# Optimization experiments

Measured on AMD Instinct MI355X. Metric: run time of the kernel, lower is better.

The kernel has to match this reference:

```python
import jax, jax.numpy as jnp
from jax import lax
import numpy as np

EPS = 1e-5
K = 12
S = 32  # sample_point


def sq_dist(q, p):
    # q: [b,m,3], p: [b,n,3] -> [b,m,n]
    return (jnp.sum(q * q, -1)[..., None]
            - 2.0 * jnp.einsum('bmc,bnc->bmn', q, p)
            + jnp.sum(p * p, -1)[:, None, :])


def fps(xyz, m):
    # furthest point sampling, starts at index 0 (matches pointnet2_utils)
    b, n, _ = xyz.shape
    init_idx = jnp.zeros((b,), jnp.int32)

    def step(carry, _):
        dist, last = carry  # dist [b,n], last [b]
        last_xyz = jnp.take_along_axis(xyz, last[:, None, None], axis=1)  # [b,1,3]
        d = jnp.sum((xyz - last_xyz) ** 2, -1)  # [b,n]
        dist = jnp.minimum(dist, d)
        nxt = jnp.argmax(dist, -1).astype(jnp.int32)
        return (dist, nxt), nxt

    (_, _), idxs = lax.scan(step, (jnp.full((b, n), 1e10, xyz.dtype), init_idx), None, length=m - 1)
    return jnp.concatenate([init_idx[None, :], idxs], 0).T  # [b,m]


def index_points(points, idx):
    # points [b,n,c], idx [b,...] -> [b,...,c]
    b = points.shape[0]
    flat = idx.reshape(b, -1)
    g = jnp.take_along_axis(points, flat[..., None], axis=1)
    return g.reshape(idx.shape + (points.shape[-1],))


def knn(k, xyz, new_xyz):
    d = sq_dist(new_xyz, xyz)  # [b,m,n]
    return lax.top_k(-d, k)[1]  # k smallest distances


def graph_op(grouped, W, bias, gamma, beta, mean, var):
    # grouped [b,m,k,d]; pointwise conv (kernel_size=1) + BN(eval) + ReLU + max over k
    y = jnp.einsum('bmkd,od->bmko', grouped, W) + bias
    y = (y - mean) * (gamma * lax.rsqrt(var + EPS)) + beta
    y = jnp.maximum(y, 0.0)
    return jnp.max(y, axis=2)  # [b,m,out]


def setup_inputs() -> dict:
    key = jax.random.key(0)
    ks = jax.random.split(key, 16)
    b, n = 16, 8192
    d_s, d_t, d_out = 256, 1024, 1024
    inp = {
        'feature_s': jax.random.normal(ks[0], (b, n, d_s), jnp.float32),
        'xyz_s': jax.random.uniform(ks[1], (b, n, 3), jnp.float32),
        'feature_t': jax.random.normal(ks[2], (b, n, d_t), jnp.float32),
        'xyz_t': jax.random.uniform(ks[3], (b, n, 3), jnp.float32),
        'Ws': jax.random.normal(ks[4], (d_out, d_s), jnp.float32) * 0.05,
        'bias_s': jax.random.normal(ks[5], (d_out,), jnp.float32) * 0.05,
        'gamma_s': jnp.ones((d_out,), jnp.float32),
        'beta_s': jnp.zeros((d_out,), jnp.float32),
        'mean_s': jax.random.normal(ks[6], (d_out,), jnp.float32) * 0.05,
        'var_s': jax.random.uniform(ks[7], (d_out,), jnp.float32, 0.5, 1.5),
        'Wt': jax.random.normal(ks[8], (d_out, d_t), jnp.float32) * 0.03,
        'bias_t': jax.random.normal(ks[9], (d_out,), jnp.float32) * 0.05,
        'gamma_t': jnp.ones((d_out,), jnp.float32),
        'beta_t': jnp.zeros((d_out,), jnp.float32),
        'mean_t': jax.random.normal(ks[10], (d_out,), jnp.float32) * 0.05,
        'var_t': jax.random.uniform(ks[11], (d_out,), jnp.float32, 0.5, 1.5),
    }
    return inp


def reference(feature_s, xyz_s, feature_t, xyz_t,
              Ws, bias_s, gamma_s, beta_s, mean_s, var_s,
              Wt, bias_t, gamma_t, beta_t, mean_t, var_t):
    # total_xyz defaults to xyz_t
    fps_idx = fps(xyz_t, S)                    # [b,S]
    new_xyz = index_points(xyz_t, fps_idx)     # [b,S,3]
    idx_t = knn(K, xyz_t, new_xyz)             # [b,S,K]
    grouped_t = index_points(feature_t, idx_t) # [b,S,K,1024]
    idx_s = knn(K, xyz_s, new_xyz)             # [b,S,K]
    grouped_s = index_points(feature_s, idx_s) # [b,S,K,256]
    out_s = graph_op(grouped_s, Ws, bias_s, gamma_s, beta_s, mean_s, var_s)
    out_t = graph_op(grouped_t, Wt, bias_t, gamma_t, beta_t, mean_t, var_t)
    return (out_s, out_t)
```

## Files before the change

### kernel.cpp

```cpp
#include <hip/hip_runtime.h>
#include <hip/hip_bf16.h>


#define NPTS 8192
#define SPTS 32
#define KNN_K 12
#define DS 256
#define DT 1024
#define DOUT 1024

typedef float f32x4 __attribute__((ext_vector_type(4)));
typedef __bf16 bf16x8 __attribute__((ext_vector_type(8)));
typedef unsigned short ushort_t;
typedef unsigned long long u64;

__device__ __forceinline__ ushort_t f2bf(float f) {
    unsigned int u = __float_as_uint(f);
    u += 0x7fffu + ((u >> 16) & 1u);
    return (ushort_t)(u >> 16);
}

__global__ __launch_bounds__(512) void fps_convw_kernel(const float* __restrict__ xyz,
                                                        float* __restrict__ new_xyz,
                                                        const float* __restrict__ Wt,
                                                        ushort_t* __restrict__ Wb_t,
                                                        const float* __restrict__ Ws,
                                                        ushort_t* __restrict__ Wb_s) {
    int bid = blockIdx.x;
    int tid = threadIdx.x;

    if (bid >= 16) {
        int lin = (bid - 16) * 512 + tid;
        const int stride = 240 * 512;
        for (int i = lin; i < (DT * DOUT) / 4; i += stride) {
            int col = i >> 8, k4 = i & 255;
            float4 v = reinterpret_cast<const float4*>(Wt)[i];
            ushort4 u;
            u.x = f2bf(v.x); u.y = f2bf(v.y); u.z = f2bf(v.z); u.w = f2bf(v.w);
            size_t off = (size_t)(k4 >> 3) * (DOUT * 32) + col * 32 + (k4 & 7) * 4;
            *reinterpret_cast<ushort4*>(Wb_t + off) = u;
        }
        for (int i = lin; i < (DS * DOUT) / 4; i += stride) {
            int col = i >> 6, k4 = i & 63;
            float4 v = reinterpret_cast<const float4*>(Ws)[i];
            ushort4 u;
            u.x = f2bf(v.x); u.y = f2bf(v.y); u.z = f2bf(v.z); u.w = f2bf(v.w);
            size_t off = (size_t)(k4 >> 3) * (DOUT * 32) + col * 32 + (k4 & 7) * 4;
            *reinterpret_cast<ushort4*>(Wb_s + off) = u;
        }
        return;
    }

    {
#pragma clang fp contract(off)
        int b = bid;
        const float* base = xyz + (size_t)b * NPTS * 3;

        __shared__ float cx[NPTS], cy[NPTS], cz[NPTS];
        __shared__ u64 rkey[2][8];

        float px[16], py[16], pz[16], dd[16];
#pragma unroll
        for (int i = 0; i < 16; ++i) {
            int p = tid + i * 512;
            px[i] = base[p * 3 + 0];
            py[i] = base[p * 3 + 1];
            pz[i] = base[p * 3 + 2];
            dd[i] = 1e10f;
            cx[p] = px[i]; cy[p] = py[i]; cz[p] = pz[i];
        }

        float lx = base[0], ly = base[1], lz = base[2];
        if (tid == 0) {
            new_xyz[((size_t)b * SPTS + 0) * 3 + 0] = lx;
            new_xyz[((size_t)b * SPTS + 0) * 3 + 1] = ly;
            new_xyz[((size_t)b * SPTS + 0) * 3 + 2] = lz;
        }

        int w = tid >> 6;
        for (int it = 1; it < SPTS; ++it) {
            int par = it & 1;
            u64 bk = 0;
#pragma unroll
            for (int i = 0; i < 16; ++i) {
                float dx = px[i] - lx, dy = py[i] - ly, dz = pz[i] - lz;
                float d = dx * dx + dy * dy;
                d = d + dz * dz;
                float nd = fminf(dd[i], d);
                dd[i] = nd;
                u64 kd = ((u64)__float_as_uint(nd) << 32) | (unsigned)(8191 - (tid + i * 512));
                bk = (kd > bk) ? kd : bk;
            }
#pragma unroll
            for (int off = 1; off < 64; off <<= 1) {
                u64 ok = __shfl_xor(bk, off);
                bk = (ok > bk) ? ok : bk;
            }
            if ((tid & 63) == 0) rkey[par][w] = bk;
            __syncthreads();
            u64 nk = rkey[par][0];
#pragma unroll
            for (int w2 = 1; w2 < 8; ++w2) {
                u64 v2 = rkey[par][w2];
                nk = (v2 > nk) ? v2 : nk;
            }
            int idx = 8191 - (int)(unsigned)(nk & 0xFFFFFFFFull);
            lx = cx[idx]; ly = cy[idx]; lz = cz[idx];
            if (tid == 0) {
                new_xyz[((size_t)b * SPTS + it) * 3 + 0] = lx;
                new_xyz[((size_t)b * SPTS + it) * 3 + 1] = ly;
                new_xyz[((size_t)b * SPTS + it) * 3 + 2] = lz;
            }
        }
    }
}

__global__ __launch_bounds__(512) void knn_kernel(const float* __restrict__ xyz_s,
                                                  const float* __restrict__ xyz_t,
                                                  const float* __restrict__ new_xyz,
                                                  int* __restrict__ idx_s,
                                                  int* __restrict__ idx_t) {
#pragma clang fp contract(off)
    int q = blockIdx.x;
    int tid = threadIdx.x;
    int w = tid >> 6, lane = tid & 63;
    int set = w >> 2;
    int sw = w & 3;
    int b = q >> 5;

    const float* pts = (set ? xyz_t : xyz_s) + (size_t)b * NPTS * 3;

    float qx = new_xyz[q * 3 + 0];
    float qy = new_xyz[q * 3 + 1];
    float qz = new_xyz[q * 3 + 2];
    float qq = qx * qx + qy * qy;
    qq = qq + qz * qz;

    u64 bd[12];
#pragma unroll
    for (int j = 0; j < 12; ++j) bd[j] = ~0ULL;

    for (int i = 0; i < 2048 / 64; ++i) {
        int p = sw * 2048 + i * 64 + lane;
        float p0 = pts[p * 3 + 0], p1 = pts[p * 3 + 1], p2 = pts[p * 3 + 2];
        float pp = p0 * p0 + p1 * p1; pp = pp + p2 * p2;
        float dot = qx * p0 + qy * p1; dot = dot + qz * p2;
        float d = (qq - 2.0f * dot) + pp;
        unsigned u = __float_as_uint(d);
        u = (u & 0x80000000u) ? ~u : (u | 0x80000000u);
        u64 key = ((u64)u << 32) | (unsigned)p;
        if (key < bd[11]) {
#pragma unroll
            for (int j = 11; j > 0; --j) {
                bool keep = (key >= bd[j]);
                u64 sh = (key >= bd[j - 1]) ? key : bd[j - 1];
                bd[j] = keep ? bd[j] : sh;
            }
            if (key < bd[0]) bd[0] = key;
        }
    }

    __shared__ u64 sd[2][48];

#pragma unroll
    for (int r = 0; r < KNN_K; ++r) {
        u64 cv = bd[0];
#pragma unroll
        for (int off = 1; off < 64; off <<= 1) {
            u64 ov = __shfl_xor(cv, off);
            cv = (ov < cv) ? ov : cv;
        }
        if (lane == 0) sd[set][sw * KNN_K + r] = cv;
        if (cv == bd[0]) {
#pragma unroll
            for (int j = 0; j < 11; ++j) bd[j] = bd[j + 1];
            bd[11] = ~0ULL;
        }
    }
    __syncthreads();

    if (sw == 0) {
        int* outp = (set ? idx_t : idx_s) + q * KNN_K;
        u64 cd = (lane < 48) ? sd[set][lane] : ~0ULL;
#pragma unroll
        for (int r = 0; r < KNN_K; ++r) {
            u64 mv = cd;
#pragma unroll
            for (int off = 1; off < 64; off <<= 1) {
                u64 ov = __shfl_xor(mv, off);
                mv = (ov < mv) ? ov : mv;
            }
            if (lane == 0) outp[r] = (int)(unsigned)(mv & 0xFFFFFFFFull);
            if (cd == mv) cd = ~0ULL;
        }
    }
}

template <int KD>
__device__ __forceinline__ void gemm_body(int mblk, int ch, const float* __restrict__ feat,
                                          const int* __restrict__ idx,
                                          const ushort_t* __restrict__ Wb,
                                          const float* __restrict__ bias,
                                          const float* __restrict__ gamma,
                                          const float* __restrict__ beta,
                                          const float* __restrict__ mean,
                                          const float* __restrict__ var,
                                          float* __restrict__ out,
                                          ushort_t (*abuf)[64][40]) {
    const int NK = KD / 32;
    int tid = threadIdx.x;
    int w = tid >> 6, lane = tid & 63;
    int lrow = lane & 15, kgrp = lane >> 4;

    int r = tid >> 3, seg = tid & 7;
    int q = mblk * 4 + (r >> 4);
    int k = r & 15;
    bool valid = (k < KNN_K);
    int b = q >> 5;
    int src = valid ? idx[q * KNN_K + k] : 0;
    const float* srcp = feat + ((size_t)b * NPTS + src) * KD + seg * 4;

    f32x4 acc[4][4];
#pragma unroll
    for (int mi = 0; mi < 4; ++mi)
#pragma unroll
        for (int ni = 0; ni < 4; ++ni) {
            f32x4 z = {0.f, 0.f, 0.f, 0.f};
            acc[mi][ni] = z;
        }

    {
        float4 v = {0.f, 0.f, 0.f, 0.f};
        if (valid) v = *reinterpret_cast<const float4*>(srcp);
        ushort4 u;
        u.x = f2bf(v.x); u.y = f2bf(v.y); u.z = f2bf(v.z); u.w = f2bf(v.w);
        *reinterpret_cast<ushort4*>(&abuf[0][r][seg * 4]) = u;
    }
    __syncthreads();

    for (int kk = 0; kk < NK; ++kk) {
        int cur = kk & 1;
        float4 nv = {0.f, 0.f, 0.f, 0.f};
        if (kk + 1 < NK && valid)
            nv = *reinterpret_cast<const float4*>(srcp + (kk + 1) * 32);

        bf16x8 a[4];
#pragma unroll
        for (int mf = 0; mf < 4; ++mf)
            a[mf] = *reinterpret_cast<const bf16x8*>(&abuf[cur][mf * 16 + lrow][kgrp * 8]);

#pragma unroll
        for (int nf = 0; nf < 4; ++nf) {
            int col = ch * 512 + w * 64 + nf * 16 + lrow;
            const ushort_t* bp = Wb + (size_t)kk * (DOUT * 32) + (size_t)col * 32 + kgrp * 8;
            bf16x8 bfr = *reinterpret_cast<const bf16x8*>(bp);
#pragma unroll
            for (int mf = 0; mf < 4; ++mf)
                acc[mf][nf] = __builtin_amdgcn_mfma_f32_16x16x32_bf16(a[mf], bfr, acc[mf][nf], 0, 0, 0);
        }

        if (kk + 1 < NK) {
            ushort4 u;
            u.x = f2bf(nv.x); u.y = f2bf(nv.y); u.z = f2bf(nv.z); u.w = f2bf(nv.w);
            *reinterpret_cast<ushort4*>(&abuf[cur ^ 1][r][seg * 4]) = u;
        }
        __syncthreads();
    }

#pragma unroll
    for (int nf = 0; nf < 4; ++nf) {
        int col = ch * 512 + w * 64 + nf * 16 + lrow;
        float sc = gamma[col] / sqrtf(var[col] + 1e-5f);
        float sh = (bias[col] - mean[col]) * sc + beta[col];
#pragma unroll
        for (int mf = 0; mf < 4; ++mf) {
            float m;
            if (kgrp < 3) {
                float y0 = fmaxf(acc[mf][nf][0] * sc + sh, 0.0f);
                float y1 = fmaxf(acc[mf][nf][1] * sc + sh, 0.0f);
                float y2 = fmaxf(acc[mf][nf][2] * sc + sh, 0.0f);
                float y3 = fmaxf(acc[mf][nf][3] * sc + sh, 0.0f);
                m = fmaxf(fmaxf(y0, y1), fmaxf(y2, y3));
            } else {
                m = -1e30f;
            }
            m = fmaxf(m, __shfl_xor(m, 16));
            m = fmaxf(m, __shfl_xor(m, 32));
            if (kgrp == 0) out[(size_t)(mblk * 4 + mf) * DOUT + col] = m;
        }
    }
}

struct GP {
    const float* feature_s; const float* feature_t;
    const int* idx_s; const int* idx_t;
    const ushort_t* Wb_s; const ushort_t* Wb_t;
    const float* bias_s; const float* gamma_s; const float* beta_s;
    const float* mean_s; const float* var_s;
    const float* bias_t; const float* gamma_t; const float* beta_t;
    const float* mean_t; const float* var_t;
    float* out;
};

__global__ __launch_bounds__(512, 4) void gemm_kernel(GP P) {
    __shared__ ushort_t abuf[2][64][40];
    int bid = blockIdx.x;
    bool is_t = (bid < 256);
    int r2 = bid & 255;
    int mblk = r2 >> 1, ch = r2 & 1;
    if (is_t) {
        gemm_body<DT>(mblk, ch, P.feature_t, P.idx_t, P.Wb_t, P.bias_t, P.gamma_t,
                      P.beta_t, P.mean_t, P.var_t, P.out + (size_t)512 * 1024, abuf);
    } else {
        gemm_body<DS>(mblk, ch, P.feature_s, P.idx_s, P.Wb_s, P.bias_s, P.gamma_s,
                      P.beta_s, P.mean_s, P.var_s, P.out, abuf);
    }
}

extern "C" void kernel_launch(void* const* d_in, const int* in_sizes, int n_in,
                              void* d_out, int out_size, void* d_ws, size_t ws_size,
                              hipStream_t stream) {
    const float* feature_s = (const float*)d_in[0];
    const float* xyz_s     = (const float*)d_in[1];
    const float* feature_t = (const float*)d_in[2];
    const float* xyz_t     = (const float*)d_in[3];
    const float* Ws        = (const float*)d_in[4];
    const float* Wt        = (const float*)d_in[10];
    float* out = (float*)d_out;

    char* ws = (char*)d_ws;
    float* new_xyz  = (float*)(ws + 0);
    int* idx_s      = (int*)(ws + 8192);
    int* idx_t      = (int*)(ws + 32768);
    ushort_t* Wb_s  = (ushort_t*)(ws + 57344);
    ushort_t* Wb_t  = (ushort_t*)(ws + 581632);

    fps_convw_kernel<<<256, 512, 0, stream>>>(xyz_t, new_xyz, Wt, Wb_t, Ws, Wb_s);
    knn_kernel<<<512, 512, 0, stream>>>(xyz_s, xyz_t, new_xyz, idx_s, idx_t);

    GP P;
    P.feature_s = feature_s; P.feature_t = feature_t;
    P.idx_s = idx_s; P.idx_t = idx_t;
    P.Wb_s = Wb_s; P.Wb_t = Wb_t;
    P.bias_s = (const float*)d_in[5];  P.gamma_s = (const float*)d_in[6];
    P.beta_s = (const float*)d_in[7];  P.mean_s  = (const float*)d_in[8];
    P.var_s  = (const float*)d_in[9];
    P.bias_t = (const float*)d_in[11]; P.gamma_t = (const float*)d_in[12];
    P.beta_t = (const float*)d_in[13]; P.mean_t  = (const float*)d_in[14];
    P.var_t  = (const float*)d_in[15];
    P.out = out;

    gemm_kernel<<<512, 512, 0, stream>>>(P);
}
```

Baseline: 108.6 us.

## Restructure grouped GEMM to one query per block without shared memory staging

The GEMM kernel now gives each block one query and a 256-column slice, and each wave loads its 12 gathered feature rows straight from global memory into MFMA A fragments. This removes the LDS double buffer and the block-wide syncs. Conversion to bf16 now uses the packed v_cvt_pk_bf16_f32 instruction, and the grid grows to 4096 blocks of 256 threads. In exchange, weight fragments are no longer reused across four queries, so weight traffic rises about fourfold and A rows are reloaded by every wave and column tile.

```diff
diff --git a/kernel.cpp b/kernel.cpp
--- a/kernel.cpp
+++ b/kernel.cpp
@@ -197,7 +197,7 @@
 }
 
 template <int KD>
-__device__ __forceinline__ void gemm_body(int mblk, int ch, const float* __restrict__ feat,
+__device__ __forceinline__ void gemm_wave(int q, int ct, const float* __restrict__ feat,
                                           const int* __restrict__ idx,
                                           const ushort_t* __restrict__ Wb,
                                           const float* __restrict__ bias,
@@ -205,89 +205,64 @@
                                           const float* __restrict__ beta,
                                           const float* __restrict__ mean,
                                           const float* __restrict__ var,
-                                          float* __restrict__ out,
-                                          ushort_t (*abuf)[64][40]) {
+                                          float* __restrict__ out) {
     const int NK = KD / 32;
     int tid = threadIdx.x;
     int w = tid >> 6, lane = tid & 63;
     int lrow = lane & 15, kgrp = lane >> 4;
-
-    int r = tid >> 3, seg = tid & 7;
-    int q = mblk * 4 + (r >> 4);
-    int k = r & 15;
-    bool valid = (k < KNN_K);
     int b = q >> 5;
-    int src = valid ? idx[q * KNN_K + k] : 0;
-    const float* srcp = feat + ((size_t)b * NPTS + src) * KD + seg * 4;
-
-    f32x4 acc[4][4];
-#pragma unroll
-    for (int mi = 0; mi < 4; ++mi)
-#pragma unroll
-        for (int ni = 0; ni < 4; ++ni) {
-            f32x4 z = {0.f, 0.f, 0.f, 0.f};
-            acc[mi][ni] = z;
-        }
-
-    {
-        float4 v = {0.f, 0.f, 0.f, 0.f};
-        if (valid) v = *reinterpret_cast<const float4*>(srcp);
-        ushort4 u;
-        u.x = f2bf(v.x); u.y = f2bf(v.y); u.z = f2bf(v.z); u.w = f2bf(v.w);
-        *reinterpret_cast<ushort4*>(&abuf[0][r][seg * 4]) = u;
-    }
-    __syncthreads();
-
+
+    int rl = (lrow < KNN_K) ? lrow : 0;
+    int src = idx[q * KNN_K + rl];
+    const float* ap = feat + ((size_t)b * NPTS + src) * KD + kgrp * 8;
+    int colbase = ct * 256 + w * 64;
+
+    f32x4 acc[4];
+#pragma unroll
+    for (int nf = 0; nf < 4; ++nf) {
+        f32x4 z = {0.f, 0.f, 0.f, 0.f};
+        acc[nf] = z;
+    }
+
+#pragma unroll 4
     for (int kk = 0; kk < NK; ++kk) {
-        int cur = kk & 1;
-        float4 nv = {0.f, 0.f, 0.f, 0.f};
-        if (kk + 1 < NK && valid)
-            nv = *reinterpret_cast<const float4*>(srcp + (kk + 1) * 32);
-
-        bf16x8 a[4];
-#pragma unroll
-        for (int mf = 0; mf < 4; ++mf)
-            a[mf] = *reinterpret_cast<const bf16x8*>(&abuf[cur][mf * 16 + lrow][kgrp * 8]);
-
+        float4 alo = *reinterpret_cast<const float4*>(ap + kk * 32);
+        float4 ahi = *reinterpret_cast<const float4*>(ap + kk * 32 + 4);
+        unsigned w0, w1, w2, w3;
+        asm("v_cvt_pk_bf16_f32 %0, %1, %2" : "=v"(w0) : "v"(alo.x), "v"(alo.y));
+        asm("v_cvt_pk_bf16_f32 %0, %1, %2" : "=v"(w1) : "v"(alo.z), "v"(alo.w));
+        asm("v_cvt_pk_bf16_f32 %0, %1, %2" : "=v"(w2) : "v"(ahi.x), "v"(ahi.y));
+        asm("v_cvt_pk_bf16_f32 %0, %1, %2" : "=v"(w3) : "v"(ahi.z), "v"(ahi.w));
+        union { unsigned u[4]; bf16x8 v; } au;
+        au.u[0] = w0; au.u[1] = w1; au.u[2] = w2; au.u[3] = w3;
+        bf16x8 af = au.v;
+
+        const ushort_t* bp = Wb + (size_t)kk * (DOUT * 32) + (size_t)(colbase + lrow) * 32 + kgrp * 8;
 #pragma unroll
         for (int nf = 0; nf < 4; ++nf) {
-            int col = ch * 512 + w * 64 + nf * 16 + lrow;
-            const ushort_t* bp = Wb + (size_t)kk * (DOUT * 32) + (size_t)col * 32 + kgrp * 8;
-            bf16x8 bfr = *reinterpret_cast<const bf16x8*>(bp);
-#pragma unroll
-            for (int mf = 0; mf < 4; ++mf)
-                acc[mf][nf] = __builtin_amdgcn_mfma_f32_16x16x32_bf16(a[mf], bfr, acc[mf][nf], 0, 0, 0);
-        }
-
-        if (kk + 1 < NK) {
-            ushort4 u;
-            u.x = f2bf(nv.x); u.y = f2bf(nv.y); u.z = f2bf(nv.z); u.w = f2bf(nv.w);
-            *reinterpret_cast<ushort4*>(&abuf[cur ^ 1][r][seg * 4]) = u;
-        }
-        __syncthreads();
+            bf16x8 bfr = *reinterpret_cast<const bf16x8*>(bp + nf * 512);
+            acc[nf] = __builtin_amdgcn_mfma_f32_16x16x32_bf16(af, bfr, acc[nf], 0, 0, 0);
+        }
     }
 
 #pragma unroll
     for (int nf = 0; nf < 4; ++nf) {
-        int col = ch * 512 + w * 64 + nf * 16 + lrow;
+        int col = colbase + nf * 16 + lrow;
         float sc = gamma[col] / sqrtf(var[col] + 1e-5f);
         float sh = (bias[col] - mean[col]) * sc + beta[col];
-#pragma unroll
-        for (int mf = 0; mf < 4; ++mf) {
-            float m;
-            if (kgrp < 3) {
-                float y0 = fmaxf(acc[mf][nf][0] * sc + sh, 0.0f);
-                float y1 = fmaxf(acc[mf][nf][1] * sc + sh, 0.0f);
-                float y2 = fmaxf(acc[mf][nf][2] * sc + sh, 0.0f);
-                float y3 = fmaxf(acc[mf][nf][3] * sc + sh, 0.0f);
-                m = fmaxf(fmaxf(y0, y1), fmaxf(y2, y3));
-            } else {
-                m = -1e30f;
-            }
-            m = fmaxf(m, __shfl_xor(m, 16));
-            m = fmaxf(m, __shfl_xor(m, 32));
-            if (kgrp == 0) out[(size_t)(mblk * 4 + mf) * DOUT + col] = m;
-        }
+        float m;
+        if (kgrp < 3) {
+            float y0 = fmaxf(acc[nf][0] * sc + sh, 0.0f);
+            float y1 = fmaxf(acc[nf][1] * sc + sh, 0.0f);
+            float y2 = fmaxf(acc[nf][2] * sc + sh, 0.0f);
+            float y3 = fmaxf(acc[nf][3] * sc + sh, 0.0f);
+            m = fmaxf(fmaxf(y0, y1), fmaxf(y2, y3));
+        } else {
+            m = -1e30f;
+        }
+        m = fmaxf(m, __shfl_xor(m, 16));
+        m = fmaxf(m, __shfl_xor(m, 32));
+        if (kgrp == 0) out[(size_t)q * DOUT + col] = m;
     }
 }
 
@@ -302,18 +277,17 @@
     float* out;
 };
 
-__global__ __launch_bounds__(512, 4) void gemm_kernel(GP P) {
-    __shared__ ushort_t abuf[2][64][40];
+__global__ __launch_bounds__(256, 6) void gemm_kernel(GP P) {
     int bid = blockIdx.x;
-    bool is_t = (bid < 256);
-    int r2 = bid & 255;
-    int mblk = r2 >> 1, ch = r2 & 1;
+    bool is_t = (bid < 2048);
+    int r2 = bid & 2047;
+    int q = r2 >> 2, ct = r2 & 3;
     if (is_t) {
-        gemm_body<DT>(mblk, ch, P.feature_t, P.idx_t, P.Wb_t, P.bias_t, P.gamma_t,
-                      P.beta_t, P.mean_t, P.var_t, P.out + (size_t)512 * 1024, abuf);
+        gemm_wave<DT>(q, ct, P.feature_t, P.idx_t, P.Wb_t, P.bias_t, P.gamma_t,
+                      P.beta_t, P.mean_t, P.var_t, P.out + (size_t)512 * 1024);
     } else {
-        gemm_body<DS>(mblk, ch, P.feature_s, P.idx_s, P.Wb_s, P.bias_s, P.gamma_s,
-                      P.beta_s, P.mean_s, P.var_s, P.out, abuf);
+        gemm_wave<DS>(q, ct, P.feature_s, P.idx_s, P.Wb_s, P.bias_s, P.gamma_s,
+                      P.beta_s, P.mean_s, P.var_s, P.out);
     }
 }
 
@@ -350,5 +324,5 @@
     P.var_t  = (const float*)d_in[15];
     P.out = out;
 
-    gemm_kernel<<<512, 512, 0, stream>>>(P);
-}
+    gemm_kernel<<<4096, 256, 0, stream>>>(P);
+}
```

Measured after the change: 209.5 us. 1.93x slower.

## Deepen gather prefetch in grouped GEMM with 4-stage 64-wide LDS pipeline

Applied to the files above, without the earlier changes.

The gather-GEMM kernel now stages 64-column chunks of gathered feature rows into a 4-slot LDS ring and keeps two register sets of float4 loads in flight, running two chunks ahead. Before, only one 32-wide chunk was prefetched per K step. Each thread now loads 16-byte segments for two rows, and LDS rows are padded to 72 to cut bank conflicts. The aim is to hide the latency of the irregular global gather behind MFMA work. In exchange it uses more registers and LDS (about 36KB per block), which may reduce occupancy under launch bounds of 4 blocks.

```diff
diff --git a/kernel.cpp b/kernel.cpp
--- a/kernel.cpp
+++ b/kernel.cpp
@@ -18,6 +18,12 @@
     unsigned int u = __float_as_uint(f);
     u += 0x7fffu + ((u >> 16) & 1u);
     return (ushort_t)(u >> 16);
+}
+
+__device__ __forceinline__ ushort4 cvt4(float4 v) {
+    ushort4 u;
+    u.x = f2bf(v.x); u.y = f2bf(v.y); u.z = f2bf(v.z); u.w = f2bf(v.w);
+    return u;
 }
 
 __global__ __launch_bounds__(512) void fps_convw_kernel(const float* __restrict__ xyz,
@@ -35,18 +41,14 @@
         for (int i = lin; i < (DT * DOUT) / 4; i += stride) {
             int col = i >> 8, k4 = i & 255;
             float4 v = reinterpret_cast<const float4*>(Wt)[i];
-            ushort4 u;
-            u.x = f2bf(v.x); u.y = f2bf(v.y); u.z = f2bf(v.z); u.w = f2bf(v.w);
             size_t off = (size_t)(k4 >> 3) * (DOUT * 32) + col * 32 + (k4 & 7) * 4;
-            *reinterpret_cast<ushort4*>(Wb_t + off) = u;
+            *reinterpret_cast<ushort4*>(Wb_t + off) = cvt4(v);
         }
         for (int i = lin; i < (DS * DOUT) / 4; i += stride) {
             int col = i >> 6, k4 = i & 63;
             float4 v = reinterpret_cast<const float4*>(Ws)[i];
-            ushort4 u;
-            u.x = f2bf(v.x); u.y = f2bf(v.y); u.z = f2bf(v.z); u.w = f2bf(v.w);
             size_t off = (size_t)(k4 >> 3) * (DOUT * 32) + col * 32 + (k4 & 7) * 4;
-            *reinterpret_cast<ushort4*>(Wb_s + off) = u;
+            *reinterpret_cast<ushort4*>(Wb_s + off) = cvt4(v);
         }
         return;
     }
@@ -197,7 +199,7 @@
 }
 
 template <int KD>
-__device__ __forceinline__ void gemm_body(int mblk, int ch, const float* __restrict__ feat,
+__device__ __forceinline__ void gemm_body(int qg, int ch, const float* __restrict__ feat,
                                           const int* __restrict__ idx,
                                           const ushort_t* __restrict__ Wb,
                                           const float* __restrict__ bias,
@@ -206,66 +208,97 @@
                                           const float* __restrict__ mean,
                                           const float* __restrict__ var,
                                           float* __restrict__ out,
-                                          ushort_t (*abuf)[64][40]) {
+                                          ushort_t (*abuf)[64][72]) {
     const int NK = KD / 32;
+    const int NS = KD / 128;
     int tid = threadIdx.x;
     int w = tid >> 6, lane = tid & 63;
     int lrow = lane & 15, kgrp = lane >> 4;
-
-    int r = tid >> 3, seg = tid & 7;
-    int q = mblk * 4 + (r >> 4);
-    int k = r & 15;
-    bool valid = (k < KNN_K);
-    int b = q >> 5;
-    int src = valid ? idx[q * KNN_K + k] : 0;
-    const float* srcp = feat + ((size_t)b * NPTS + src) * KD + seg * 4;
+    int q0 = qg * 4;
+    int b = q0 >> 5;
+
+    int sr = tid >> 4, seg = tid & 15;
+    int row0 = sr, row1 = sr + 32;
+    bool v0 = (row0 & 15) < KNN_K;
+    bool v1 = (row1 & 15) < KNN_K;
+    int src0 = v0 ? idx[(q0 + (row0 >> 4)) * KNN_K + (row0 & 15)] : 0;
+    int src1 = v1 ? idx[(q0 + (row1 >> 4)) * KNN_K + (row1 & 15)] : 0;
+    const float* sp0 = feat + ((size_t)b * NPTS + src0) * KD + seg * 4;
+    const float* sp1 = feat + ((size_t)b * NPTS + src1) * KD + seg * 4;
+
+    const float4 fz = {0.f, 0.f, 0.f, 0.f};
+
+#define ISSUE(pa, X0, X1, X2, X3)                                              \
+    do {                                                                       \
+        X0 = v0 ? *reinterpret_cast<const float4*>(sp0 + (pa) * 64) : fz;      \
+        X1 = v1 ? *reinterpret_cast<const float4*>(sp1 + (pa) * 64) : fz;      \
+        X2 = v0 ? *reinterpret_cast<const float4*>(sp0 + (pa + 1) * 64) : fz;  \
+        X3 = v1 ? *reinterpret_cast<const float4*>(sp1 + (pa + 1) * 64) : fz;  \
+    } while (0)
+
+#define WRITEP(pa, X0, X1, X2, X3)                                                    \
+    do {                                                                              \
+        *reinterpret_cast<ushort4*>(&abuf[(pa) & 3][row0][seg * 4]) = cvt4(X0);       \
+        *reinterpret_cast<ushort4*>(&abuf[(pa) & 3][row1][seg * 4]) = cvt4(X1);       \
+        *reinterpret_cast<ushort4*>(&abuf[(pa + 1) & 3][row0][seg * 4]) = cvt4(X2);   \
+        *reinterpret_cast<ushort4*>(&abuf[(pa + 1) & 3][row1][seg * 4]) = cvt4(X3);   \
+    } while (0)
 
     f32x4 acc[4][4];
 #pragma unroll
-    for (int mi = 0; mi < 4; ++mi)
-#pragma unroll
-        for (int ni = 0; ni < 4; ++ni) {
+    for (int mf = 0; mf < 4; ++mf)
+#pragma unroll
+        for (int nf = 0; nf < 4; ++nf) {
             f32x4 z = {0.f, 0.f, 0.f, 0.f};
-            acc[mi][ni] = z;
+            acc[mf][nf] = z;
         }
 
     {
-        float4 v = {0.f, 0.f, 0.f, 0.f};
-        if (valid) v = *reinterpret_cast<const float4*>(srcp);
-        ushort4 u;
-        u.x = f2bf(v.x); u.y = f2bf(v.y); u.z = f2bf(v.z); u.w = f2bf(v.w);
-        *reinterpret_cast<ushort4*>(&abuf[0][r][seg * 4]) = u;
-    }
+        float4 t0, t1, t2, t3;
+        ISSUE(0, t0, t1, t2, t3);
+        WRITEP(0, t0, t1, t2, t3);
+    }
+    float4 A0, A1, A2, A3, B0, B1, B2, B3;
+    ISSUE(2, A0, A1, A2, A3);
     __syncthreads();
 
-    for (int kk = 0; kk < NK; ++kk) {
-        int cur = kk & 1;
-        float4 nv = {0.f, 0.f, 0.f, 0.f};
-        if (kk + 1 < NK && valid)
-            nv = *reinterpret_cast<const float4*>(srcp + (kk + 1) * 32);
-
-        bf16x8 a[4];
-#pragma unroll
-        for (int mf = 0; mf < 4; ++mf)
-            a[mf] = *reinterpret_cast<const bf16x8*>(&abuf[cur][mf * 16 + lrow][kgrp * 8]);
-
-#pragma unroll
-        for (int nf = 0; nf < 4; ++nf) {
-            int col = ch * 512 + w * 64 + nf * 16 + lrow;
-            const ushort_t* bp = Wb + (size_t)kk * (DOUT * 32) + (size_t)col * 32 + kgrp * 8;
-            bf16x8 bfr = *reinterpret_cast<const bf16x8*>(bp);
+#pragma unroll
+    for (int i = 0; i < NS; ++i) {
+        if ((i & 1) == 0) {
+            if (i + 2 < NS) ISSUE(2 * i + 4, B0, B1, B2, B3);
+        } else {
+            if (i + 2 < NS) ISSUE(2 * i + 4, A0, A1, A2, A3);
+        }
+
+#pragma unroll
+        for (int kk2 = 0; kk2 < 4; ++kk2) {
+            int kk = 4 * i + kk2;
+            int pb = (kk >> 1) & 3, hf = kk & 1;
+            bf16x8 a[4];
 #pragma unroll
             for (int mf = 0; mf < 4; ++mf)
-                acc[mf][nf] = __builtin_amdgcn_mfma_f32_16x16x32_bf16(a[mf], bfr, acc[mf][nf], 0, 0, 0);
-        }
-
-        if (kk + 1 < NK) {
-            ushort4 u;
-            u.x = f2bf(nv.x); u.y = f2bf(nv.y); u.z = f2bf(nv.z); u.w = f2bf(nv.w);
-            *reinterpret_cast<ushort4*>(&abuf[cur ^ 1][r][seg * 4]) = u;
+                a[mf] = *reinterpret_cast<const bf16x8*>(
+                    &abuf[pb][mf * 16 + lrow][hf * 32 + kgrp * 8]);
+#pragma unroll
+            for (int nf = 0; nf < 4; ++nf) {
+                int col = ch * 512 + w * 64 + nf * 16 + lrow;
+                const ushort_t* bp = Wb + (size_t)kk * (DOUT * 32) + (size_t)col * 32 + kgrp * 8;
+                bf16x8 bfr = *reinterpret_cast<const bf16x8*>(bp);
+#pragma unroll
+                for (int mf = 0; mf < 4; ++mf)
+                    acc[mf][nf] = __builtin_amdgcn_mfma_f32_16x16x32_bf16(a[mf], bfr, acc[mf][nf], 0, 0, 0);
+            }
         }
         __syncthreads();
-    }
+
+        if (i + 1 < NS) {
+            if ((i & 1) == 0) WRITEP(2 * i + 2, A0, A1, A2, A3);
+            else              WRITEP(2 * i + 2, B0, B1, B2, B3);
+            __syncthreads();
+        }
+    }
+#undef ISSUE
+#undef WRITEP
 
 #pragma unroll
     for (int nf = 0; nf < 4; ++nf) {
@@ -286,7 +319,7 @@
             }
             m = fmaxf(m, __shfl_xor(m, 16));
             m = fmaxf(m, __shfl_xor(m, 32));
-            if (kgrp == 0) out[(size_t)(mblk * 4 + mf) * DOUT + col] = m;
+            if (kgrp == 0) out[(size_t)(q0 + mf) * DOUT + col] = m;
         }
     }
 }
@@ -303,16 +336,16 @@
 };
 
 __global__ __launch_bounds__(512, 4) void gemm_kernel(GP P) {
-    __shared__ ushort_t abuf[2][64][40];
+    __shared__ ushort_t abuf[4][64][72];
     int bid = blockIdx.x;
     bool is_t = (bid < 256);
-    int r2 = bid & 255;
-    int mblk = r2 >> 1, ch = r2 & 1;
+    int r2 = is_t ? bid : bid - 256;
+    int qg = r2 >> 1, ch = r2 & 1;
     if (is_t) {
-        gemm_body<DT>(mblk, ch, P.feature_t, P.idx_t, P.Wb_t, P.bias_t, P.gamma_t,
+        gemm_body<DT>(qg, ch, P.feature_t, P.idx_t, P.Wb_t, P.bias_t, P.gamma_t,
                       P.beta_t, P.mean_t, P.var_t, P.out + (size_t)512 * 1024, abuf);
     } else {
-        gemm_body<DS>(mblk, ch, P.feature_s, P.idx_s, P.Wb_s, P.bias_s, P.gamma_s,
+        gemm_body<DS>(qg, ch, P.feature_s, P.idx_s, P.Wb_s, P.bias_s, P.gamma_s,
                       P.beta_s, P.mean_s, P.var_s, P.out, abuf);
     }
 }
```

Measured after the change: 190.2 us. +75.2%, slower.

## Stage full gathered A tile in LDS and compute all output columns per block

Applied to the files above, without the earlier changes.

The GEMM kernel now has each block gather and convert the entire K-dimension of its 4 query rows (times 16 neighbors) into shared memory once, then runs the MFMA loop with no per-step barriers or double buffering. Each block covers all 1024 output columns (8 column fragments per wave) instead of splitting them across two blocks, which halves the redundant feature gathers and the block count to 256. In exchange it uses about 130KB of LDS and a larger accumulator set, which limits occupancy to one block per CU. It also loses the overlap between global loads and MFMA work.

```diff
diff --git a/kernel.cpp b/kernel.cpp
--- a/kernel.cpp
+++ b/kernel.cpp
@@ -18,6 +18,12 @@
     unsigned int u = __float_as_uint(f);
     u += 0x7fffu + ((u >> 16) & 1u);
     return (ushort_t)(u >> 16);
+}
+
+__device__ __forceinline__ ushort4 cvt4(float4 v) {
+    ushort4 u;
+    u.x = f2bf(v.x); u.y = f2bf(v.y); u.z = f2bf(v.z); u.w = f2bf(v.w);
+    return u;
 }
 
 __global__ __launch_bounds__(512) void fps_convw_kernel(const float* __restrict__ xyz,
@@ -35,18 +41,14 @@
         for (int i = lin; i < (DT * DOUT) / 4; i += stride) {
             int col = i >> 8, k4 = i & 255;
             float4 v = reinterpret_cast<const float4*>(Wt)[i];
-            ushort4 u;
-            u.x = f2bf(v.x); u.y = f2bf(v.y); u.z = f2bf(v.z); u.w = f2bf(v.w);
             size_t off = (size_t)(k4 >> 3) * (DOUT * 32) + col * 32 + (k4 & 7) * 4;
-            *reinterpret_cast<ushort4*>(Wb_t + off) = u;
+            *reinterpret_cast<ushort4*>(Wb_t + off) = cvt4(v);
         }
         for (int i = lin; i < (DS * DOUT) / 4; i += stride) {
             int col = i >> 6, k4 = i & 63;
             float4 v = reinterpret_cast<const float4*>(Ws)[i];
-            ushort4 u;
-            u.x = f2bf(v.x); u.y = f2bf(v.y); u.z = f2bf(v.z); u.w = f2bf(v.w);
             size_t off = (size_t)(k4 >> 3) * (DOUT * 32) + col * 32 + (k4 & 7) * 4;
-            *reinterpret_cast<ushort4*>(Wb_s + off) = u;
+            *reinterpret_cast<ushort4*>(Wb_s + off) = cvt4(v);
         }
         return;
     }
@@ -197,7 +199,7 @@
 }
 
 template <int KD>
-__device__ __forceinline__ void gemm_body(int mblk, int ch, const float* __restrict__ feat,
+__device__ __forceinline__ void gemm_body(int qg, const float* __restrict__ feat,
                                           const int* __restrict__ idx,
                                           const ushort_t* __restrict__ Wb,
                                           const float* __restrict__ bias,
@@ -206,70 +208,62 @@
                                           const float* __restrict__ mean,
                                           const float* __restrict__ var,
                                           float* __restrict__ out,
-                                          ushort_t (*abuf)[64][40]) {
+                                          ushort_t* __restrict__ abuf) {
     const int NK = KD / 32;
+    const int NJ = KD / 32;
+    const int STRIDE = KD + 8;
     int tid = threadIdx.x;
     int w = tid >> 6, lane = tid & 63;
     int lrow = lane & 15, kgrp = lane >> 4;
+    int q0 = qg * 4;
+    int b = q0 >> 5;
 
     int r = tid >> 3, seg = tid & 7;
-    int q = mblk * 4 + (r >> 4);
-    int k = r & 15;
-    bool valid = (k < KNN_K);
-    int b = q >> 5;
-    int src = valid ? idx[q * KNN_K + k] : 0;
+    int sk = r & 15;
+    bool valid = (sk < KNN_K);
+    int src = valid ? idx[(q0 + (r >> 4)) * KNN_K + sk] : 0;
     const float* srcp = feat + ((size_t)b * NPTS + src) * KD + seg * 4;
-
-    f32x4 acc[4][4];
-#pragma unroll
-    for (int mi = 0; mi < 4; ++mi)
-#pragma unroll
-        for (int ni = 0; ni < 4; ++ni) {
+    ushort_t* wbase = abuf + (size_t)r * STRIDE + seg * 4;
+
+    const float4 fz = {0.f, 0.f, 0.f, 0.f};
+#pragma unroll 4
+    for (int j = 0; j < NJ; ++j) {
+        float4 v = valid ? *reinterpret_cast<const float4*>(srcp + j * 32) : fz;
+        *reinterpret_cast<ushort4*>(wbase + j * 32) = cvt4(v);
+    }
+    __syncthreads();
+
+    f32x4 acc[4][8];
+#pragma unroll
+    for (int mf = 0; mf < 4; ++mf)
+#pragma unroll
+        for (int nf = 0; nf < 8; ++nf) {
             f32x4 z = {0.f, 0.f, 0.f, 0.f};
-            acc[mi][ni] = z;
-        }
-
-    {
-        float4 v = {0.f, 0.f, 0.f, 0.f};
-        if (valid) v = *reinterpret_cast<const float4*>(srcp);
-        ushort4 u;
-        u.x = f2bf(v.x); u.y = f2bf(v.y); u.z = f2bf(v.z); u.w = f2bf(v.w);
-        *reinterpret_cast<ushort4*>(&abuf[0][r][seg * 4]) = u;
-    }
-    __syncthreads();
-
+            acc[mf][nf] = z;
+        }
+
+    int colbase = w * 128;
+#pragma unroll 2
     for (int kk = 0; kk < NK; ++kk) {
-        int cur = kk & 1;
-        float4 nv = {0.f, 0.f, 0.f, 0.f};
-        if (kk + 1 < NK && valid)
-            nv = *reinterpret_cast<const float4*>(srcp + (kk + 1) * 32);
-
         bf16x8 a[4];
 #pragma unroll
         for (int mf = 0; mf < 4; ++mf)
-            a[mf] = *reinterpret_cast<const bf16x8*>(&abuf[cur][mf * 16 + lrow][kgrp * 8]);
-
-#pragma unroll
-        for (int nf = 0; nf < 4; ++nf) {
-            int col = ch * 512 + w * 64 + nf * 16 + lrow;
+            a[mf] = *reinterpret_cast<const bf16x8*>(
+                abuf + (size_t)(mf * 16 + lrow) * STRIDE + kk * 32 + kgrp * 8);
+#pragma unroll
+        for (int nf = 0; nf < 8; ++nf) {
+            int col = colbase + nf * 16 + lrow;
             const ushort_t* bp = Wb + (size_t)kk * (DOUT * 32) + (size_t)col * 32 + kgrp * 8;
             bf16x8 bfr = *reinterpret_cast<const bf16x8*>(bp);
 #pragma unroll
             for (int mf = 0; mf < 4; ++mf)
                 acc[mf][nf] = __builtin_amdgcn_mfma_f32_16x16x32_bf16(a[mf], bfr, acc[mf][nf], 0, 0, 0);
         }
-
-        if (kk + 1 < NK) {
-            ushort4 u;
-            u.x = f2bf(nv.x); u.y = f2bf(nv.y); u.z = f2bf(nv.z); u.w = f2bf(nv.w);
-            *reinterpret_cast<ushort4*>(&abuf[cur ^ 1][r][seg * 4]) = u;
-        }
-        __syncthreads();
-    }
-
-#pragma unroll
-    for (int nf = 0; nf < 4; ++nf) {
-        int col = ch * 512 + w * 64 + nf * 16 + lrow;
+    }
+
+#pragma unroll
+    for (int nf = 0; nf < 8; ++nf) {
+        int col = colbase + nf * 16 + lrow;
         float sc = gamma[col] / sqrtf(var[col] + 1e-5f);
         float sh = (bias[col] - mean[col]) * sc + beta[col];
 #pragma unroll
@@ -286,7 +280,7 @@
             }
             m = fmaxf(m, __shfl_xor(m, 16));
             m = fmaxf(m, __shfl_xor(m, 32));
-            if (kgrp == 0) out[(size_t)(mblk * 4 + mf) * DOUT + col] = m;
+            if (kgrp == 0) out[(size_t)(q0 + mf) * DOUT + col] = m;
         }
     }
 }
@@ -302,17 +296,14 @@
     float* out;
 };
 
-__global__ __launch_bounds__(512, 4) void gemm_kernel(GP P) {
-    __shared__ ushort_t abuf[2][64][40];
+__global__ __launch_bounds__(512, 1) void gemm_kernel(GP P) {
+    __shared__ ushort_t abuf[64 * (DT + 8)];
     int bid = blockIdx.x;
-    bool is_t = (bid < 256);
-    int r2 = bid & 255;
-    int mblk = r2 >> 1, ch = r2 & 1;
-    if (is_t) {
-        gemm_body<DT>(mblk, ch, P.feature_t, P.idx_t, P.Wb_t, P.bias_t, P.gamma_t,
+    if (bid < 128) {
+        gemm_body<DT>(bid, P.feature_t, P.idx_t, P.Wb_t, P.bias_t, P.gamma_t,
                       P.beta_t, P.mean_t, P.var_t, P.out + (size_t)512 * 1024, abuf);
     } else {
-        gemm_body<DS>(mblk, ch, P.feature_s, P.idx_s, P.Wb_s, P.bias_s, P.gamma_s,
+        gemm_body<DS>(bid - 128, P.feature_s, P.idx_s, P.Wb_s, P.bias_s, P.gamma_s,
                       P.beta_s, P.mean_s, P.var_s, P.out, abuf);
     }
 }
@@ -350,5 +341,5 @@
     P.var_t  = (const float*)d_in[15];
     P.out = out;
 
-    gemm_kernel<<<512, 512, 0, stream>>>(P);
-}
+    gemm_kernel<<<256, 512, 0, stream>>>(P);
+}
```

Result: slower. 139.4 us (+28.4%).
